# Optimization experiments

Measured on AMD Instinct MI355X. Metric: run time of the kernel, lower is better.

Reference implementation:

```python
import jax, jax.numpy as jnp
import numpy as np

QUERY_DIM = 3072
HEADS = 24
HEAD_DIM = 128
INNER = HEADS * HEAD_DIM  # 3072
MLP_HIDDEN = int(QUERY_DIM * 4.0)  # 12288
MLP_MULT = 2
EPS = 1e-5
B, S = 1, 4096


def setup_inputs() -> dict:
    key = jax.random.key(0)
    ks = jax.random.split(key, 8)
    hidden_states = jax.random.normal(ks[0], (B, S, QUERY_DIM), dtype=jnp.float32)
    # rotary angles for half the head dim (interleaved / non-neox style)
    t = jnp.arange(S, dtype=jnp.float32)[:, None]
    inv_freq = 1.0 / (10000.0 ** (jnp.arange(0, HEAD_DIM, 2, dtype=jnp.float32) / HEAD_DIM))
    ang = t * inv_freq[None, :]
    cos = jnp.cos(ang)
    sin = jnp.sin(ang)
    W_qkv_mlp = jax.random.normal(ks[1], (QUERY_DIM, 3 * INNER + MLP_HIDDEN * MLP_MULT), dtype=jnp.float32) * 0.02
    W_out = jax.random.normal(ks[2], (INNER + MLP_HIDDEN, QUERY_DIM), dtype=jnp.float32) * 0.02
    b_out = jnp.zeros((QUERY_DIM,), dtype=jnp.float32)
    norm_q_w = jnp.ones((HEAD_DIM,), dtype=jnp.float32)
    norm_k_w = jnp.ones((HEAD_DIM,), dtype=jnp.float32)
    return {"hidden_states": hidden_states, "cos": cos, "sin": sin,
            "W_qkv_mlp": W_qkv_mlp, "W_out": W_out, "b_out": b_out,
            "norm_q_w": norm_q_w, "norm_k_w": norm_k_w}


def _rmsnorm(x, w, eps=EPS):
    var = jnp.mean(jnp.square(x), axis=-1, keepdims=True)
    return x * jax.lax.rsqrt(var + eps) * w


def _rope_interleaved(x, cos, sin):
    # x: [B,S,H,D]; cos/sin: [S, D//2]. Non-neox: rotate interleaved pairs.
    x1 = x[..., 0::2]
    x2 = x[..., 1::2]
    c = cos[None, :, None, :]
    s = sin[None, :, None, :]
    o1 = x1 * c - x2 * s
    o2 = x2 * c + x1 * s
    return jnp.stack([o1, o2], axis=-1).reshape(x.shape)


def reference(hidden_states, cos, sin, W_qkv_mlp, W_out, b_out, norm_q_w, norm_k_w):
    h = hidden_states @ W_qkv_mlp  # [B,S, 3*INNER + 2*MLP_HIDDEN]
    qkv, mlp = jnp.split(h, [3 * INNER], axis=-1)
    q, k, v = jnp.split(qkv, 3, axis=-1)
    q = q.reshape(B, S, HEADS, HEAD_DIM)
    k = k.reshape(B, S, HEADS, HEAD_DIM)
    v = v.reshape(B, S, HEADS, HEAD_DIM)
    q = _rmsnorm(q, norm_q_w)
    k = _rmsnorm(k, norm_k_w)
    q = _rope_interleaved(q, cos, sin)
    k = _rope_interleaved(k, cos, sin)
    scale = 1.0 / np.sqrt(HEAD_DIM)
    scores = jnp.einsum('bqhd,bkhd->bhqk', q, k) * scale
    probs = jax.nn.softmax(scores, axis=-1)
    attn = jnp.einsum('bhqk,bkhd->bqhd', probs, v)
    attn = attn.reshape(B, S, INNER)
    m1, m2 = jnp.split(mlp, 2, axis=-1)
    mlp_out = jax.nn.silu(m1) * m2
    out = jnp.concatenate([attn, mlp_out], axis=-1) @ W_out + b_out
    return out
```

## Files before the change

kernel.cpp:

```cpp
#include <hip/hip_runtime.h>

typedef short shortx8 __attribute__((ext_vector_type(8)));
typedef float floatx4 __attribute__((ext_vector_type(4)));
typedef unsigned short u16;

#define GLB(x) ((const __attribute__((address_space(1))) void*)(x))
#define LDSC(x) ((__attribute__((address_space(3))) void*)(x))
#define BAR() asm volatile("s_barrier" ::: "memory")
#define WAITV8() asm volatile("s_waitcnt vmcnt(8)" ::: "memory")

__device__ __forceinline__ float bf2f(u16 u) {
  unsigned x = ((unsigned)u) << 16;
  float f;
  __builtin_memcpy(&f, &x, 4);
  return f;
}
__device__ __forceinline__ u16 f2bf(float f) {
  unsigned x;
  __builtin_memcpy(&x, &f, 4);
  x += 0x7fffu + ((x >> 16) & 1u);
  return (u16)(x >> 16);
}

__global__ __launch_bounds__(256) void cast_bf16(const float* __restrict__ src,
                                                 u16* __restrict__ dst) {
  const size_t i = ((size_t)blockIdx.x * 256 + threadIdx.x) << 3;
  floatx4 a = *(const floatx4*)(src + i);
  floatx4 b = *(const floatx4*)(src + i + 4);
  shortx8 o;
#pragma unroll
  for (int e = 0; e < 4; ++e) {
    o[e] = (short)f2bf(a[e]);
    o[e + 4] = (short)f2bf(b[e]);
  }
  *(shortx8*)(dst + i) = o;
}

__global__ __launch_bounds__(256) void transpose_cast(const float* __restrict__ src,
                                                      u16* __restrict__ dst,
                                                      int R, int C) {
  __shared__ u16 T[64 * 72];
  const int tiles_c = C >> 6;
  const int r0 = (blockIdx.x / tiles_c) << 6;
  const int c0 = (blockIdx.x % tiles_c) << 6;
  const int tid = threadIdx.x;
  const int rl = tid >> 4;
  const int cb = (tid & 15) << 2;
#pragma unroll
  for (int rr = 0; rr < 4; ++rr) {
    const int row = rr * 16 + rl;
    floatx4 v = *(const floatx4*)(src + (size_t)(r0 + row) * C + c0 + cb);
#pragma unroll
    for (int i = 0; i < 4; ++i) T[(cb + i) * 72 + row] = f2bf(v[i]);
  }
  __syncthreads();
#pragma unroll
  for (int ii = 0; ii < 2; ++ii) {
    const int chunk = tid + (ii << 8);
    const int cr = chunk >> 3;
    const int r8 = (chunk & 7) << 3;
    shortx8 v = *(const shortx8*)(T + cr * 72 + r8);
    *(shortx8*)(dst + (size_t)(c0 + cr) * R + r0 + r8) = v;
  }
}

template <int MODE>
__global__ __launch_bounds__(512, 2) void gemm8(const u16* __restrict__ A,
                                                const u16* __restrict__ B,
                                                void* __restrict__ Cout,
                                                int M, int N, int K, int Ksub) {
  __shared__ u16 lds[8 * 8192];

  const int nbm = M >> 8;
  const int nwg = nbm * (N >> 8);
  const int cpx = nwg >> 3;
  const int wg = ((int)blockIdx.x & 7) * cpx + ((int)blockIdx.x >> 3);
  const int bm = wg % nbm;
  const int bn = wg / nbm;
  const int koff = (int)blockIdx.y * Ksub;

  const int tid = threadIdx.x;
  const int lane = tid & 63;
  const int w = tid >> 6;
  const int wm = w >> 2;
  const int wn = w & 3;
  const int l15 = lane & 15;
  const int l4 = lane >> 4;
  const int NT = Ksub >> 6;

  const int lrow = lane >> 2;
  const int lblk = lane & 3;

#define UNIT(buf, mat, ks) (lds + (((buf) * 4 + (mat) * 2 + (ks)) << 13))

  const u16* Abase = A + (size_t)bm * 256 * K + koff;
  const u16* Bbase = B + (size_t)bn * 256 * K + koff;

  auto STAGE = [&](int mat, int ks, int buf, int t) {
    const u16* gb = mat ? Bbase : Abase;
#pragma unroll
    for (int j = 0; j < 2; ++j) {
      const int row = (w * 2 + j) * 16 + lrow;
      const int sblk = lblk ^ ((row >> 1) & 3);
      const u16* src = gb + (size_t)row * K + (t << 6) + (ks << 5) + (sblk << 3);
      __builtin_amdgcn_global_load_lds(GLB(src),
                                       LDSC(UNIT(buf, mat, ks) + ((w * 2 + j) << 9)),
                                       16, 0, 0);
    }
  };
  auto LDA = [&](int mf, int ks, int buf) -> shortx8 {
    const int row = wm * 128 + mf * 16 + l15;
    return *(const shortx8*)(UNIT(buf, 0, ks) + row * 32 + ((l4 ^ ((row >> 1) & 3)) << 3));
  };
  auto LDB = [&](int nf, int ks, int buf) -> shortx8 {
    const int row = wn * 64 + nf * 16 + l15;
    return *(const shortx8*)(UNIT(buf, 1, ks) + row * 32 + ((l4 ^ ((row >> 1) & 3)) << 3));
  };

  floatx4 acc[8][4] = {};

  STAGE(0, 0, 0, 0); STAGE(1, 0, 0, 0);
  STAGE(0, 1, 0, 0); STAGE(1, 1, 0, 0);
  STAGE(0, 0, 1, 1); STAGE(1, 0, 1, 1);
  WAITV8();
  BAR();

#pragma unroll 2
  for (int T = 0; T < NT; ++T) {
    const int cur = T & 1, nxt = cur ^ 1;
    const int t1 = (T + 1 < NT) ? T + 1 : NT - 1;
    const int t2 = (T + 2 < NT) ? T + 2 : NT - 1;
    shortx8 af[4], bf[4];

#pragma unroll
    for (int m = 0; m < 4; ++m) af[m] = LDA(m, 0, cur);
#pragma unroll
    for (int n = 0; n < 4; ++n) bf[n] = LDB(n, 0, cur);
    STAGE(0, 1, nxt, t1);
    BAR();
    __builtin_amdgcn_s_setprio(1);
#pragma unroll
    for (int m = 0; m < 4; ++m)
#pragma unroll
      for (int n = 0; n < 4; ++n)
        acc[m][n] = __builtin_amdgcn_mfma_f32_16x16x32_bf16(af[m], bf[n], acc[m][n], 0, 0, 0);
    __builtin_amdgcn_s_setprio(0);
    BAR();

#pragma unroll
    for (int m = 0; m < 4; ++m) af[m] = LDA(4 + m, 0, cur);
    STAGE(1, 1, nxt, t1);
    BAR();
    __builtin_amdgcn_s_setprio(1);
#pragma unroll
    for (int m = 0; m < 4; ++m)
#pragma unroll
      for (int n = 0; n < 4; ++n)
        acc[4 + m][n] = __builtin_amdgcn_mfma_f32_16x16x32_bf16(af[m], bf[n], acc[4 + m][n], 0, 0, 0);
    __builtin_amdgcn_s_setprio(0);
    WAITV8();
    BAR();

#pragma unroll
    for (int m = 0; m < 4; ++m) af[m] = LDA(m, 1, cur);
#pragma unroll
    for (int n = 0; n < 4; ++n) bf[n] = LDB(n, 1, cur);
    STAGE(0, 0, cur, t2);
    BAR();
    __builtin_amdgcn_s_setprio(1);
#pragma unroll
    for (int m = 0; m < 4; ++m)
#pragma unroll
      for (int n = 0; n < 4; ++n)
        acc[m][n] = __builtin_amdgcn_mfma_f32_16x16x32_bf16(af[m], bf[n], acc[m][n], 0, 0, 0);
    __builtin_amdgcn_s_setprio(0);
    BAR();

#pragma unroll
    for (int m = 0; m < 4; ++m) af[m] = LDA(4 + m, 1, cur);
    STAGE(1, 0, cur, t2);
    BAR();
    __builtin_amdgcn_s_setprio(1);
#pragma unroll
    for (int m = 0; m < 4; ++m)
#pragma unroll
      for (int n = 0; n < 4; ++n)
        acc[4 + m][n] = __builtin_amdgcn_mfma_f32_16x16x32_bf16(af[m], bf[n], acc[4 + m][n], 0, 0, 0);
    __builtin_amdgcn_s_setprio(0);
    WAITV8();
    BAR();
  }

  const int orow0 = bm * 256 + wm * 128 + (l4 << 2);
  const int ocol0 = bn * 256 + wn * 64 + l15;
  if (MODE == 0) {
    u16* C = (u16*)Cout;
#pragma unroll
    for (int m = 0; m < 8; ++m)
#pragma unroll
      for (int n = 0; n < 4; ++n)
#pragma unroll
        for (int r = 0; r < 4; ++r)
          C[(size_t)(orow0 + m * 16 + r) * N + ocol0 + n * 16] = f2bf(acc[m][n][r]);
  } else {
    float* C = (float*)Cout + (size_t)blockIdx.y * M * N;
#pragma unroll
    for (int m = 0; m < 8; ++m)
#pragma unroll
      for (int n = 0; n < 4; ++n)
#pragma unroll
        for (int r = 0; r < 4; ++r)
          C[(size_t)(orow0 + m * 16 + r) * N + ocol0 + n * 16] = acc[m][n][r];
  }
}
#undef UNIT

__global__ __launch_bounds__(256) void reduce_bias(const float* __restrict__ P,
                                                   const float* __restrict__ bias,
                                                   float* __restrict__ out) {
  const size_t base = ((size_t)blockIdx.x * 256 + threadIdx.x) << 2;
  const size_t stride = (size_t)4096 * 3072;
  floatx4 a = *(const floatx4*)(P + base);
  floatx4 b = *(const floatx4*)(P + stride + base);
  floatx4 c = *(const floatx4*)(P + 2 * stride + base);
  floatx4 d = *(const floatx4*)(P + 3 * stride + base);
  floatx4 bb = *(const floatx4*)(bias + (base % 3072));
  *(floatx4*)(out + base) = a + b + c + d + bb;
}

#define QSCALE (0.08838834764831845f * 1.4426950408889634f)

__global__ __launch_bounds__(256, 2) void qkv_prep(
    const u16* __restrict__ H, const float* __restrict__ cosb,
    const float* __restrict__ sinb, const float* __restrict__ nqw,
    const float* __restrict__ nkw, u16* __restrict__ Qo, u16* __restrict__ Ko,
    u16* __restrict__ Vo) {
  __shared__ u16 VT[128 * 72];
  const int head = blockIdx.y;
  const int t0 = blockIdx.x << 6;
  const int tid = threadIdx.x;
  const int tl = tid >> 2;
  const int db = (tid & 3) << 5;
  const int token = t0 + tl;

  const u16* hp = H + (size_t)token * 33792 + head * 128 + db;
  shortx8 qv[4], kvv[4], vv[4];
#pragma unroll
  for (int i = 0; i < 4; ++i) {
    qv[i] = *(const shortx8*)(hp + i * 8);
    kvv[i] = *(const shortx8*)(hp + 3072 + i * 8);
    vv[i] = *(const shortx8*)(hp + 6144 + i * 8);
  }
  float qx[32], kx[32];
  float sq = 0.f, sk = 0.f;
#pragma unroll
  for (int i = 0; i < 4; ++i)
#pragma unroll
    for (int j = 0; j < 8; ++j) {
      float a = bf2f((u16)qv[i][j]); qx[i * 8 + j] = a; sq += a * a;
      float b = bf2f((u16)kvv[i][j]); kx[i * 8 + j] = b; sk += b * b;
    }
  sq += __shfl_xor(sq, 1); sq += __shfl_xor(sq, 2);
  sk += __shfl_xor(sk, 1); sk += __shfl_xor(sk, 2);
  const float rq = rsqrtf(sq * (1.0f / 128.0f) + 1e-5f);
  const float rk = rsqrtf(sk * (1.0f / 128.0f) + 1e-5f);

  shortx8 oqv[4], okv[4];
#pragma unroll
  for (int p = 0; p < 16; ++p) {
    const float c = cosb[(size_t)token * 64 + (db >> 1) + p];
    const float s = sinb[(size_t)token * 64 + (db >> 1) + p];
    const int vi = p >> 2, vj = (p & 3) << 1;
    float a1 = qx[2 * p] * rq * nqw[db + 2 * p];
    float a2 = qx[2 * p + 1] * rq * nqw[db + 2 * p + 1];
    oqv[vi][vj] = (short)f2bf((a1 * c - a2 * s) * QSCALE);
    oqv[vi][vj + 1] = (short)f2bf((a2 * c + a1 * s) * QSCALE);
    float b1 = kx[2 * p] * rk * nkw[db + 2 * p];
    float b2 = kx[2 * p + 1] * rk * nkw[db + 2 * p + 1];
    okv[vi][vj] = (short)f2bf(b1 * c - b2 * s);
    okv[vi][vj + 1] = (short)f2bf(b2 * c + b1 * s);
  }
  {
    u16* qo = Qo + (size_t)head * 4096 * 128 + (size_t)token * 128 + db;
    u16* ko = Ko + (size_t)head * 4096 * 128 + (size_t)token * 128 + db;
#pragma unroll
    for (int i = 0; i < 4; ++i) {
      *(shortx8*)(qo + i * 8) = oqv[i];
      *(shortx8*)(ko + i * 8) = okv[i];
    }
  }
#pragma unroll
  for (int i = 0; i < 4; ++i)
#pragma unroll
    for (int j = 0; j < 8; ++j) VT[(db + i * 8 + j) * 72 + tl] = (u16)vv[i][j];
  __syncthreads();
#pragma unroll
  for (int ii = 0; ii < 4; ++ii) {
    const int chunk = tid + (ii << 8);
    const int d = chunk >> 3;
    const int j8 = (chunk & 7) << 3;
    shortx8 v = *(const shortx8*)(VT + d * 72 + j8);
    *(shortx8*)(Vo + (size_t)head * 128 * 4096 + (size_t)d * 4096 + t0 + j8) = v;
  }
}

__global__ __launch_bounds__(256) void mlp_act(const u16* __restrict__ H,
                                               u16* __restrict__ CC) {
  const size_t id = (size_t)blockIdx.x * 256 + threadIdx.x;
  const int t = (int)(id / 1536);
  const int j = ((int)(id % 1536)) << 3;
  const u16* base = H + (size_t)t * 33792;
  shortx8 a = *(const shortx8*)(base + 9216 + j);
  shortx8 b = *(const shortx8*)(base + 21504 + j);
  shortx8 o;
#pragma unroll
  for (int e = 0; e < 8; ++e) {
    float x = bf2f((u16)a[e]);
    float y = bf2f((u16)b[e]);
    float sg = 1.0f / (1.0f + exp2f(-1.4426950408889634f * x));
    o[e] = (short)f2bf(x * sg * y);
  }
  *(shortx8*)(CC + (size_t)t * 15360 + 3072 + j) = o;
}

__global__ __launch_bounds__(256, 2) void attn_kernel(const u16* __restrict__ Qg,
                                                      const u16* __restrict__ Kg,
                                                      const u16* __restrict__ Vg,
                                                      u16* __restrict__ CC) {
  __shared__ u16 Ks[128 * 128];
  __shared__ u16 Vs[128 * 128];
  __shared__ u16 Ps[4 * 16 * 128];

  const int head = blockIdx.y;
  const int q0 = blockIdx.x << 6;
  const int tid = threadIdx.x;
  const int lane = tid & 63;
  const int wave = tid >> 6;
  const int l15 = lane & 15;
  const int l4 = lane >> 4;

  const u16* Qh = Qg + (size_t)head * 4096 * 128;
  const u16* Kh = Kg + (size_t)head * 4096 * 128;
  const u16* Vh = Vg + (size_t)head * 128 * 4096;

  shortx8 qf[4];
  {
    const u16* qp = Qh + (size_t)(q0 + wave * 16 + l15) * 128 + l4 * 8;
#pragma unroll
    for (int ks = 0; ks < 4; ++ks) qf[ks] = *(const shortx8*)(qp + ks * 32);
  }

  floatx4 o[8] = {};
  float mrun[4], lrun[4];
#pragma unroll
  for (int r = 0; r < 4; ++r) { mrun[r] = -1e30f; lrun[r] = 0.0f; }

  u16* Pw = Ps + wave * 2048;
  const int swz = l15 & 7;

  for (int s0 = 0; s0 < 4096; s0 += 128) {
#pragma unroll
    for (int i = 0; i < 8; ++i) {
      const int c = wave * 8 + i;
      const int row = c * 4 + (lane >> 4);
      const int blk = (lane & 15) ^ (row & 7);
      __builtin_amdgcn_global_load_lds(GLB(Kh + (size_t)(s0 + row) * 128 + blk * 8),
                                       LDSC(Ks + c * 512), 16, 0, 0);
    }
#pragma unroll
    for (int i = 0; i < 8; ++i) {
      const int c = wave * 8 + i;
      const int row = c * 4 + (lane >> 4);
      const int blk = (lane & 15) ^ (row & 7);
      __builtin_amdgcn_global_load_lds(GLB(Vh + (size_t)row * 4096 + s0 + blk * 8),
                                       LDSC(Vs + c * 512), 16, 0, 0);
    }
    __syncthreads();

    floatx4 s[8];
    __builtin_amdgcn_s_setprio(1);
#pragma unroll
    for (int n = 0; n < 8; ++n) {
      const int krow = n * 16 + l15;
      floatx4 acc = {};
#pragma unroll
      for (int ks = 0; ks < 4; ++ks) {
        shortx8 kf = *(const shortx8*)(Ks + krow * 128 + (((ks * 4 + l4) ^ swz) << 3));
        acc = __builtin_amdgcn_mfma_f32_16x16x32_bf16(qf[ks], kf, acc, 0, 0, 0);
      }
      s[n] = acc;
    }
    __builtin_amdgcn_s_setprio(0);

    float alpha[4];
#pragma unroll
    for (int r = 0; r < 4; ++r) {
      float v = fmaxf(fmaxf(fmaxf(s[0][r], s[1][r]), fmaxf(s[2][r], s[3][r])),
                      fmaxf(fmaxf(s[4][r], s[5][r]), fmaxf(s[6][r], s[7][r])));
      v = fmaxf(v, __shfl_xor(v, 1));
      v = fmaxf(v, __shfl_xor(v, 2));
      v = fmaxf(v, __shfl_xor(v, 4));
      v = fmaxf(v, __shfl_xor(v, 8));
      const float mn = fmaxf(mrun[r], v);
      alpha[r] = exp2f(mrun[r] - mn);
      mrun[r] = mn;
    }

    float rs[4] = {0.f, 0.f, 0.f, 0.f};
#pragma unroll
    for (int n = 0; n < 8; ++n) {
#pragma unroll
      for (int r = 0; r < 4; ++r) {
        const float p = exp2f(s[n][r] - mrun[r]);
        rs[r] += p;
        const int prow = (l4 << 2) + r;
        const int pblk = ((n << 1) + (l15 >> 3)) ^ (prow & 7);
        Pw[prow * 128 + (pblk << 3) + (l15 & 7)] = f2bf(p);
      }
    }
#pragma unroll
    for (int r = 0; r < 4; ++r) {
      float v = rs[r];
      v += __shfl_xor(v, 1);
      v += __shfl_xor(v, 2);
      v += __shfl_xor(v, 4);
      v += __shfl_xor(v, 8);
      lrun[r] = lrun[r] * alpha[r] + v;
    }
    if (__any((alpha[0] < 1.0f) || (alpha[1] < 1.0f) ||
              (alpha[2] < 1.0f) || (alpha[3] < 1.0f))) {
#pragma unroll
      for (int nd = 0; nd < 8; ++nd)
#pragma unroll
        for (int r = 0; r < 4; ++r) o[nd][r] *= alpha[r];
    }

    shortx8 pf[4];
#pragma unroll
    for (int ks = 0; ks < 4; ++ks)
      pf[ks] = *(const shortx8*)(Pw + l15 * 128 + (((ks * 4 + l4) ^ swz) << 3));
    __builtin_amdgcn_s_setprio(1);
#pragma unroll
    for (int nd = 0; nd < 8; ++nd) {
      const int vrow = nd * 16 + l15;
#pragma unroll
      for (int ks = 0; ks < 4; ++ks) {
        shortx8 vf = *(const shortx8*)(Vs + vrow * 128 + (((ks * 4 + l4) ^ swz) << 3));
        o[nd] = __builtin_amdgcn_mfma_f32_16x16x32_bf16(pf[ks], vf, o[nd], 0, 0, 0);
      }
    }
    __builtin_amdgcn_s_setprio(0);
    __syncthreads();
  }

#pragma unroll
  for (int r = 0; r < 4; ++r) {
    const float inv = 1.0f / lrun[r];
    const int row = q0 + wave * 16 + (l4 << 2) + r;
    u16* outp = CC + (size_t)row * 15360 + head * 128 + l15;
#pragma unroll
    for (int nd = 0; nd < 8; ++nd) outp[nd << 4] = f2bf(o[nd][r] * inv);
  }
}

extern "C" void kernel_launch(void* const* d_in, const int* in_sizes, int n_in,
                              void* d_out, int out_size, void* d_ws, size_t ws_size,
                              hipStream_t stream) {
  const float* hs = (const float*)d_in[0];
  const float* cosb = (const float*)d_in[1];
  const float* sinb = (const float*)d_in[2];
  const float* w1 = (const float*)d_in[3];
  const float* wout = (const float*)d_in[4];
  const float* bout = (const float*)d_in[5];
  const float* nqw = (const float*)d_in[6];
  const float* nkw = (const float*)d_in[7];
  float* out = (float*)d_out;

  char* ws = (char*)d_ws;
  u16* X16 = (u16*)ws; ws += (size_t)4096 * 3072 * 2;
  u16* W1T = (u16*)ws; ws += (size_t)33792 * 3072 * 2;
  u16* WOT = (u16*)ws; ws += (size_t)3072 * 15360 * 2;
  u16* H   = (u16*)ws; ws += (size_t)4096 * 33792 * 2;
  u16* Qb  = (u16*)ws; ws += (size_t)24 * 4096 * 128 * 2;
  u16* Kb  = (u16*)ws; ws += (size_t)24 * 4096 * 128 * 2;
  u16* VTb = (u16*)ws; ws += (size_t)24 * 4096 * 128 * 2;
  u16* CC  = (u16*)ws; ws += (size_t)4096 * 15360 * 2;
  float* Pk = (float*)H;

  cast_bf16<<<6144, 256, 0, stream>>>(hs, X16);
  transpose_cast<<<(3072 / 64) * (33792 / 64), 256, 0, stream>>>(w1, W1T, 3072, 33792);
  transpose_cast<<<(15360 / 64) * (3072 / 64), 256, 0, stream>>>(wout, WOT, 15360, 3072);
  gemm8<0><<<(4096 / 256) * (33792 / 256), 512, 0, stream>>>(X16, W1T, H,
                                                             4096, 33792, 3072, 3072);
  qkv_prep<<<dim3(64, 24), 256, 0, stream>>>(H, cosb, sinb, nqw, nkw, Qb, Kb, VTb);
  mlp_act<<<(4096 * 12288 / 8) / 256, 256, 0, stream>>>(H, CC);
  attn_kernel<<<dim3(64, 24), 256, 0, stream>>>(Qb, Kb, VTb, CC);
  gemm8<1><<<dim3((4096 / 256) * (3072 / 256), 4), 512, 0, stream>>>(
      CC, WOT, Pk, 4096, 3072, 15360, 3840);
  reduce_bias<<<(4096 * 3072 / 4) / 256, 256, 0, stream>>>(Pk, bout, out);
}
```

Measured before the change: 1.958 ms.

## Simplify GEMM mainloop to K=32 double buffering with one barrier per step

The GEMM pipeline goes from a 64-wide K tile split into two 32-wide sub-stages with a deeper prefetch to a plain double-buffered 32-wide K step. Each step issues all A and B loads for the next tile at once, runs both MFMA halves, then waits for all loads and hits a single barrier. LDS use is halved, which could allow more occupancy. In exchange prefetch depth shrinks and every step fully drains outstanding memory loads, so load latency may be less hidden.

```diff
diff --git a/kernel.cpp b/kernel.cpp
--- a/kernel.cpp
+++ b/kernel.cpp
@@ -7,7 +7,7 @@
 #define GLB(x) ((const __attribute__((address_space(1))) void*)(x))
 #define LDSC(x) ((__attribute__((address_space(3))) void*)(x))
 #define BAR() asm volatile("s_barrier" ::: "memory")
-#define WAITV8() asm volatile("s_waitcnt vmcnt(8)" ::: "memory")
+#define WAITV0() asm volatile("s_waitcnt vmcnt(0)" ::: "memory")
 
 __device__ __forceinline__ float bf2f(u16 u) {
   unsigned x = ((unsigned)u) << 16;
@@ -69,7 +69,7 @@
                                                 const u16* __restrict__ B,
                                                 void* __restrict__ Cout,
                                                 int M, int N, int K, int Ksub) {
-  __shared__ u16 lds[8 * 8192];
+  __shared__ u16 lds[4 * 8192];
 
   const int nbm = M >> 8;
   const int nwg = nbm * (N >> 8);
@@ -86,58 +86,55 @@
   const int wn = w & 3;
   const int l15 = lane & 15;
   const int l4 = lane >> 4;
-  const int NT = Ksub >> 6;
+  const int NT = Ksub >> 5;
 
   const int lrow = lane >> 2;
   const int lblk = lane & 3;
 
-#define UNIT(buf, mat, ks) (lds + (((buf) * 4 + (mat) * 2 + (ks)) << 13))
+#define UNIT(buf, mat) (lds + (((buf) * 2 + (mat)) << 13))
 
   const u16* Abase = A + (size_t)bm * 256 * K + koff;
   const u16* Bbase = B + (size_t)bn * 256 * K + koff;
 
-  auto STAGE = [&](int mat, int ks, int buf, int t) {
+  auto STAGE = [&](int mat, int buf, int t) {
     const u16* gb = mat ? Bbase : Abase;
 #pragma unroll
     for (int j = 0; j < 2; ++j) {
       const int row = (w * 2 + j) * 16 + lrow;
       const int sblk = lblk ^ ((row >> 1) & 3);
-      const u16* src = gb + (size_t)row * K + (t << 6) + (ks << 5) + (sblk << 3);
+      const u16* src = gb + (size_t)row * K + (t << 5) + (sblk << 3);
       __builtin_amdgcn_global_load_lds(GLB(src),
-                                       LDSC(UNIT(buf, mat, ks) + ((w * 2 + j) << 9)),
+                                       LDSC(UNIT(buf, mat) + ((w * 2 + j) << 9)),
                                        16, 0, 0);
     }
   };
-  auto LDA = [&](int mf, int ks, int buf) -> shortx8 {
+  auto LDA = [&](int mf, int buf) -> shortx8 {
     const int row = wm * 128 + mf * 16 + l15;
-    return *(const shortx8*)(UNIT(buf, 0, ks) + row * 32 + ((l4 ^ ((row >> 1) & 3)) << 3));
+    return *(const shortx8*)(UNIT(buf, 0) + row * 32 + ((l4 ^ ((row >> 1) & 3)) << 3));
   };
-  auto LDB = [&](int nf, int ks, int buf) -> shortx8 {
+  auto LDB = [&](int nf, int buf) -> shortx8 {
     const int row = wn * 64 + nf * 16 + l15;
-    return *(const shortx8*)(UNIT(buf, 1, ks) + row * 32 + ((l4 ^ ((row >> 1) & 3)) << 3));
+    return *(const shortx8*)(UNIT(buf, 1) + row * 32 + ((l4 ^ ((row >> 1) & 3)) << 3));
   };
 
   floatx4 acc[8][4] = {};
 
-  STAGE(0, 0, 0, 0); STAGE(1, 0, 0, 0);
-  STAGE(0, 1, 0, 0); STAGE(1, 1, 0, 0);
-  STAGE(0, 0, 1, 1); STAGE(1, 0, 1, 1);
-  WAITV8();
+  STAGE(0, 0, 0); STAGE(1, 0, 0);
+  WAITV0();
   BAR();
 
 #pragma unroll 2
   for (int T = 0; T < NT; ++T) {
     const int cur = T & 1, nxt = cur ^ 1;
     const int t1 = (T + 1 < NT) ? T + 1 : NT - 1;
-    const int t2 = (T + 2 < NT) ? T + 2 : NT - 1;
     shortx8 af[4], bf[4];
 
 #pragma unroll
-    for (int m = 0; m < 4; ++m) af[m] = LDA(m, 0, cur);
-#pragma unroll
-    for (int n = 0; n < 4; ++n) bf[n] = LDB(n, 0, cur);
-    STAGE(0, 1, nxt, t1);
-    BAR();
+    for (int m = 0; m < 4; ++m) af[m] = LDA(m, cur);
+#pragma unroll
+    for (int n = 0; n < 4; ++n) bf[n] = LDB(n, cur);
+    STAGE(0, nxt, t1);
+    STAGE(1, nxt, t1);
     __builtin_amdgcn_s_setprio(1);
 #pragma unroll
     for (int m = 0; m < 4; ++m)
@@ -145,12 +142,9 @@
       for (int n = 0; n < 4; ++n)
         acc[m][n] = __builtin_amdgcn_mfma_f32_16x16x32_bf16(af[m], bf[n], acc[m][n], 0, 0, 0);
     __builtin_amdgcn_s_setprio(0);
-    BAR();
-
-#pragma unroll
-    for (int m = 0; m < 4; ++m) af[m] = LDA(4 + m, 0, cur);
-    STAGE(1, 1, nxt, t1);
-    BAR();
+
+#pragma unroll
+    for (int m = 0; m < 4; ++m) af[m] = LDA(4 + m, cur);
     __builtin_amdgcn_s_setprio(1);
 #pragma unroll
     for (int m = 0; m < 4; ++m)
@@ -158,36 +152,8 @@
       for (int n = 0; n < 4; ++n)
         acc[4 + m][n] = __builtin_amdgcn_mfma_f32_16x16x32_bf16(af[m], bf[n], acc[4 + m][n], 0, 0, 0);
     __builtin_amdgcn_s_setprio(0);
-    WAITV8();
-    BAR();
-
-#pragma unroll
-    for (int m = 0; m < 4; ++m) af[m] = LDA(m, 1, cur);
-#pragma unroll
-    for (int n = 0; n < 4; ++n) bf[n] = LDB(n, 1, cur);
-    STAGE(0, 0, cur, t2);
-    BAR();
-    __builtin_amdgcn_s_setprio(1);
-#pragma unroll
-    for (int m = 0; m < 4; ++m)
-#pragma unroll
-      for (int n = 0; n < 4; ++n)
-        acc[m][n] = __builtin_amdgcn_mfma_f32_16x16x32_bf16(af[m], bf[n], acc[m][n], 0, 0, 0);
-    __builtin_amdgcn_s_setprio(0);
-    BAR();
-
-#pragma unroll
-    for (int m = 0; m < 4; ++m) af[m] = LDA(4 + m, 1, cur);
-    STAGE(1, 0, cur, t2);
-    BAR();
-    __builtin_amdgcn_s_setprio(1);
-#pragma unroll
-    for (int m = 0; m < 4; ++m)
-#pragma unroll
-      for (int n = 0; n < 4; ++n)
-        acc[4 + m][n] = __builtin_amdgcn_mfma_f32_16x16x32_bf16(af[m], bf[n], acc[4 + m][n], 0, 0, 0);
-    __builtin_amdgcn_s_setprio(0);
-    WAITV8();
+
+    WAITV0();
     BAR();
   }
 
```

After: 2.140 ms. 9.3% more time.

## Fuse SiLU-gated MLP activation into first GEMM epilogue via interleaved weight columns

Applied to the files above, without the earlier changes.

The transpose of W_qkv_mlp now permutes the MLP columns so that each 256-wide output tile holds matching m1 and m2 halves. The first GEMM's epilogue swaps m2 through LDS, applies silu(m1)*m2 and writes bf16 straight into the concat buffer, which removes the separate mlp_act kernel. H now stores only the 9216 QKV columns, so the large intermediate write and re-read of the MLP activations go away. In exchange the epilogue gains an extra LDS round trip and barrier, and the MLP tiles write half as many columns.

```diff
diff --git a/kernel.cpp b/kernel.cpp
--- a/kernel.cpp
+++ b/kernel.cpp
@@ -38,7 +38,7 @@
 
 __global__ __launch_bounds__(256) void transpose_cast(const float* __restrict__ src,
                                                       u16* __restrict__ dst,
-                                                      int R, int C) {
+                                                      int R, int C, int perm) {
   __shared__ u16 T[64 * 72];
   const int tiles_c = C >> 6;
   const int r0 = (blockIdx.x / tiles_c) << 6;
@@ -54,13 +54,18 @@
     for (int i = 0; i < 4; ++i) T[(cb + i) * 72 + row] = f2bf(v[i]);
   }
   __syncthreads();
+  int dbase = c0;
+  if (perm && c0 >= 9216) {
+    if (c0 < 21504) { const int u = c0 - 9216;  dbase = 9216 + ((u >> 7) << 8) + (u & 64); }
+    else            { const int u = c0 - 21504; dbase = 9216 + ((u >> 7) << 8) + 128 + (u & 64); }
+  }
 #pragma unroll
   for (int ii = 0; ii < 2; ++ii) {
     const int chunk = tid + (ii << 8);
     const int cr = chunk >> 3;
     const int r8 = (chunk & 7) << 3;
     shortx8 v = *(const shortx8*)(T + cr * 72 + r8);
-    *(shortx8*)(dst + (size_t)(c0 + cr) * R + r0 + r8) = v;
+    *(shortx8*)(dst + (size_t)(dbase + cr) * R + r0 + r8) = v;
   }
 }
 
@@ -68,6 +73,7 @@
 __global__ __launch_bounds__(512, 2) void gemm8(const u16* __restrict__ A,
                                                 const u16* __restrict__ B,
                                                 void* __restrict__ Cout,
+                                                u16* __restrict__ CC2,
                                                 int M, int N, int K, int Ksub) {
   __shared__ u16 lds[8 * 8192];
 
@@ -192,18 +198,51 @@
   }
 
   const int orow0 = bm * 256 + wm * 128 + (l4 << 2);
-  const int ocol0 = bn * 256 + wn * 64 + l15;
   if (MODE == 0) {
-    u16* C = (u16*)Cout;
-#pragma unroll
-    for (int m = 0; m < 8; ++m)
-#pragma unroll
-      for (int n = 0; n < 4; ++n)
-#pragma unroll
-        for (int r = 0; r < 4; ++r)
-          C[(size_t)(orow0 + m * 16 + r) * N + ocol0 + n * 16] = f2bf(acc[m][n][r]);
+    if (bn < 36) {
+      u16* C = (u16*)Cout;
+      const int ocol0 = bn * 256 + wn * 64 + l15;
+#pragma unroll
+      for (int m = 0; m < 8; ++m)
+#pragma unroll
+        for (int n = 0; n < 4; ++n)
+#pragma unroll
+          for (int r = 0; r < 4; ++r)
+            C[(size_t)(orow0 + m * 16 + r) * 9216 + ocol0 + n * 16] = f2bf(acc[m][n][r]);
+    } else {
+      __syncthreads();
+      float* lbuf = (float*)lds;
+      const int pairblk = wm * 2 + (wn & 1);
+      if (wn >= 2) {
+        float* dst = lbuf + pairblk * 8192;
+#pragma unroll
+        for (int m = 0; m < 8; ++m)
+#pragma unroll
+          for (int n = 0; n < 4; ++n)
+#pragma unroll
+            for (int r = 0; r < 4; ++r)
+              dst[(m * 16 + (l4 << 2) + r) * 64 + n * 16 + l15] = acc[m][n][r];
+      }
+      __syncthreads();
+      if (wn < 2) {
+        const float* src = lbuf + pairblk * 8192;
+        const int gcol0 = 3072 + (bn - 36) * 128 + wn * 64 + l15;
+#pragma unroll
+        for (int m = 0; m < 8; ++m)
+#pragma unroll
+          for (int n = 0; n < 4; ++n)
+#pragma unroll
+            for (int r = 0; r < 4; ++r) {
+              const float m1 = acc[m][n][r];
+              const float m2 = src[(m * 16 + (l4 << 2) + r) * 64 + n * 16 + l15];
+              const float sg = 1.0f / (1.0f + exp2f(-1.4426950408889634f * m1));
+              CC2[(size_t)(orow0 + m * 16 + r) * 15360 + gcol0 + n * 16] = f2bf(m1 * sg * m2);
+            }
+      }
+    }
   } else {
     float* C = (float*)Cout + (size_t)blockIdx.y * M * N;
+    const int ocol0 = bn * 256 + wn * 64 + l15;
 #pragma unroll
     for (int m = 0; m < 8; ++m)
 #pragma unroll
@@ -243,7 +282,7 @@
   const int db = (tid & 3) << 5;
   const int token = t0 + tl;
 
-  const u16* hp = H + (size_t)token * 33792 + head * 128 + db;
+  const u16* hp = H + (size_t)token * 9216 + head * 128 + db;
   shortx8 qv[4], kvv[4], vv[4];
 #pragma unroll
   for (int i = 0; i < 4; ++i) {
@@ -304,25 +343,6 @@
   }
 }
 
-__global__ __launch_bounds__(256) void mlp_act(const u16* __restrict__ H,
-                                               u16* __restrict__ CC) {
-  const size_t id = (size_t)blockIdx.x * 256 + threadIdx.x;
-  const int t = (int)(id / 1536);
-  const int j = ((int)(id % 1536)) << 3;
-  const u16* base = H + (size_t)t * 33792;
-  shortx8 a = *(const shortx8*)(base + 9216 + j);
-  shortx8 b = *(const shortx8*)(base + 21504 + j);
-  shortx8 o;
-#pragma unroll
-  for (int e = 0; e < 8; ++e) {
-    float x = bf2f((u16)a[e]);
-    float y = bf2f((u16)b[e]);
-    float sg = 1.0f / (1.0f + exp2f(-1.4426950408889634f * x));
-    o[e] = (short)f2bf(x * sg * y);
-  }
-  *(shortx8*)(CC + (size_t)t * 15360 + 3072 + j) = o;
-}
-
 __global__ __launch_bounds__(256, 2) void attn_kernel(const u16* __restrict__ Qg,
                                                       const u16* __restrict__ Kg,
                                                       const u16* __restrict__ Vg,
@@ -485,17 +505,17 @@
   u16* Kb  = (u16*)ws; ws += (size_t)24 * 4096 * 128 * 2;
   u16* VTb = (u16*)ws; ws += (size_t)24 * 4096 * 128 * 2;
   u16* CC  = (u16*)ws; ws += (size_t)4096 * 15360 * 2;
-  float* Pk = (float*)H;
+  float* Pk = (float*)(H + (size_t)4096 * 9216);
+  Pk = (float*)H;
 
   cast_bf16<<<6144, 256, 0, stream>>>(hs, X16);
-  transpose_cast<<<(3072 / 64) * (33792 / 64), 256, 0, stream>>>(w1, W1T, 3072, 33792);
-  transpose_cast<<<(15360 / 64) * (3072 / 64), 256, 0, stream>>>(wout, WOT, 15360, 3072);
-  gemm8<0><<<(4096 / 256) * (33792 / 256), 512, 0, stream>>>(X16, W1T, H,
+  transpose_cast<<<(3072 / 64) * (33792 / 64), 256, 0, stream>>>(w1, W1T, 3072, 33792, 1);
+  transpose_cast<<<(15360 / 64) * (3072 / 64), 256, 0, stream>>>(wout, WOT, 15360, 3072, 0);
+  gemm8<0><<<(4096 / 256) * (33792 / 256), 512, 0, stream>>>(X16, W1T, H, CC,
                                                              4096, 33792, 3072, 3072);
   qkv_prep<<<dim3(64, 24), 256, 0, stream>>>(H, cosb, sinb, nqw, nkw, Qb, Kb, VTb);
-  mlp_act<<<(4096 * 12288 / 8) / 256, 256, 0, stream>>>(H, CC);
   attn_kernel<<<dim3(64, 24), 256, 0, stream>>>(Qb, Kb, VTb, CC);
   gemm8<1><<<dim3((4096 / 256) * (3072 / 256), 4), 512, 0, stream>>>(
-      CC, WOT, Pk, 4096, 3072, 15360, 3840);
+      CC, WOT, Pk, nullptr, 4096, 3072, 15360, 3840);
   reduce_bias<<<(4096 * 3072 / 4) / 256, 256, 0, stream>>>(Pk, bout, out);
 }
```

New measurement: 1.934 ms. About the same (-1.2%).
